# Kernel optimization log

Measured on AMD Instinct MI355X. Metric: run time of the kernel, lower is better.

Reference implementation:

```python
import jax, jax.numpy as jnp
import numpy as np

TEMPERATURE = 8.0  # sqrt(d_k) with d_k = 64
NEG_INF = -1e30    # finite stand-in for -inf; exp() underflows to 0 identically


def _skew(s):
    # Music-Transformer relative-position skew: F.pad(s,(1,0)).view(-1,L+1,L)[:,1:,:]
    B, L, _ = s.shape
    s = jnp.pad(s, ((0, 0), (0, 0), (1, 0)))  # [B, L, L+1]
    return s.reshape(B, L + 1, L)[:, 1:, :]   # [B, L, L]


def setup_inputs() -> dict:
    key = jax.random.key(0)
    kq, kk, kv, ke = jax.random.split(key, 4)
    B, L, D = 16, 2048, 64
    q = jax.random.normal(kq, (B, L, D), dtype=jnp.float32)
    k = jax.random.normal(kk, (B, L, D), dtype=jnp.float32)
    v = jax.random.normal(kv, (B, L, D), dtype=jnp.float32)
    e = jax.random.normal(ke, (B, L, D), dtype=jnp.float32)
    # causal mask (True = masked out), broadcast to batch
    mask = jnp.broadcast_to(jnp.triu(jnp.ones((L, L), dtype=bool), k=1), (B, L, L))
    return {"q": q, "k": k, "v": v, "e": e, "mask": mask}


def reference(q, k, v, e, mask):
    attn = jnp.einsum('bqd,bkd->bqk', q, k)          # q @ k^T
    attn = attn + _skew(jnp.einsum('bqd,bkd->bqk', q, e))
    attn = attn / TEMPERATURE
    attn = jnp.where(mask, NEG_INF, attn)
    attn = jax.nn.softmax(attn, axis=2)
    attn = jnp.where(mask, 0.0, attn)
    # dropout is identity in eval mode
    output = jnp.einsum('bqk,bkd->bqd', attn, v)
    return (output, attn)
```

## Files before the change

### kernel.cpp

```cpp
#include <hip/hip_runtime.h>

typedef unsigned int u32;
typedef __fp16 h2 __attribute__((ext_vector_type(2)));
typedef _Float16 f16x8 __attribute__((ext_vector_type(8)));
typedef float f32x4 __attribute__((ext_vector_type(4)));

#define BB 16
#define LL 2048
#define DD 64
#define RPB 16
#define NTHREADS 512
#define NBLK (LL / RPB)

__device__ __forceinline__ h2 pk(float x, float y) {
#if __has_builtin(__builtin_amdgcn_cvt_pkrtz)
    return __builtin_amdgcn_cvt_pkrtz(x, y);
#else
    h2 r; r.x = (__fp16)x; r.y = (__fp16)y; return r;
#endif
}

union F8U { f16x8 v; h2 p[4]; };
__device__ __forceinline__ f16x8 pack8(float4 a, float4 b) {
    F8U u;
    u.p[0] = pk(a.x, a.y); u.p[1] = pk(a.z, a.w);
    u.p[2] = pk(b.x, b.y); u.p[3] = pk(b.z, b.w);
    return u.v;
}

#define MFMA(A, B, C) __builtin_amdgcn_mfma_f32_16x16x32_f16((A), (B), (C), 0, 0, 0)

__device__ __forceinline__ int swc(int rl, int c) { return c ^ ((rl & 7) << 3); }

__global__ __launch_bounds__(NTHREADS, 4) void attn_fused(
    const float* __restrict__ qg, const float* __restrict__ kg,
    const float* __restrict__ vg, const float* __restrict__ eg,
    float* __restrict__ out_o, float* __restrict__ out_attn)
{
    __shared__ __fp16 S_h[RPB][LL];
    __shared__ float  maxF[RPB][132];
    __shared__ float  linv[RPB];

    const int tid  = threadIdx.x;
    const int wave = tid >> 6;
    const int lane = tid & 63;
    const int o4   = lane >> 4;
    const int lc   = lane & 15;
    const int b    = blockIdx.x / NBLK;
    const int r0   = (blockIdx.x % NBLK) * RPB;
    const int nT   = (r0 >> 6) + 1;

    const float* qb = qg + (size_t)b * LL * DD;
    const float* kb = kg + (size_t)b * LL * DD;
    const float* eb = eg + (size_t)b * LL * DD;
    const float* vb = vg + (size_t)b * LL * DD;

    f16x8 qa0, qa1;
    {
        const float* qr = qb + (size_t)(r0 + lc) * DD + 8 * o4;
        float4 a0 = *(const float4*)(qr);
        float4 a1 = *(const float4*)(qr + 4);
        float4 b0 = *(const float4*)(qr + 32);
        float4 b1 = *(const float4*)(qr + 36);
        qa0 = pack8(a0, a1);
        qa1 = pack8(b0, b1);
    }

    float mx[4] = {-60000.f, -60000.f, -60000.f, -60000.f};

    const int span = r0 + 15 - (wave << 4);
    const int nTw  = (span >= 0) ? ((span >> 7) + 1) : 0;

    for (int t = 0; t < nTw; ++t) {
        const int c0w = (t << 7) + (wave << 4);

        const float* kr = kb + (size_t)(c0w + lc) * DD + 8 * o4;
        float4 k0 = *(const float4*)(kr);
        float4 k1 = *(const float4*)(kr + 4);
        float4 k2 = *(const float4*)(kr + 32);
        float4 k3 = *(const float4*)(kr + 36);

        const int j0w = c0w + 2032 - r0;
        int er0 = j0w + lc;      if (er0 > LL - 1) er0 = LL - 1;
        int er1 = j0w + 16 + lc; if (er1 > LL - 1) er1 = LL - 1;
        const float* e0p = eb + (size_t)er0 * DD + 8 * o4;
        const float* e1p = eb + (size_t)er1 * DD + 8 * o4;
        float4 ea0 = *(const float4*)(e0p);
        float4 ea1 = *(const float4*)(e0p + 4);
        float4 ea2 = *(const float4*)(e0p + 32);
        float4 ea3 = *(const float4*)(e0p + 36);
        float4 eb0 = *(const float4*)(e1p);
        float4 eb1 = *(const float4*)(e1p + 4);
        float4 eb2 = *(const float4*)(e1p + 32);
        float4 eb3 = *(const float4*)(e1p + 36);

        f16x8 kf0 = pack8(k0, k1), kf1 = pack8(k2, k3);
        f16x8 ef00 = pack8(ea0, ea1), ef01 = pack8(ea2, ea3);
        f16x8 ef10 = pack8(eb0, eb1), ef11 = pack8(eb2, eb3);

        const f32x4 z = {0.f, 0.f, 0.f, 0.f};
        f32x4 dk = MFMA(qa0, kf0, z);  dk = MFMA(qa1, kf1, dk);
        f32x4 g0 = MFMA(qa0, ef00, z); g0 = MFMA(qa1, ef01, g0);
        f32x4 g1 = MFMA(qa0, ef10, z); g1 = MFMA(qa1, ef11, g1);

#pragma unroll
        for (int i = 0; i < 4; ++i) {
            const int rl  = 4 * o4 + i;
            const int lj  = lc + 15 - rl;
            const int src = (o4 << 4) | (lj & 15);
            float ga = __shfl(g0[i], src, 64);
            float gb = __shfl(g1[i], src, 64);
            float gv = (lj < 16) ? ga : gb;
            float s = (dk[i] + gv) * 0.125f;
            const int c = c0w + lc;
            if (c > r0 + rl) s = -60000.f;
            mx[i] = fmaxf(mx[i], s);
            S_h[rl][swc(rl, c)] = (__fp16)s;
        }
    }

#pragma unroll
    for (int i = 0; i < 4; ++i)
        maxF[4 * o4 + i][(wave << 4) | lc] = mx[i];
    __syncthreads();

    for (int rr = 0; rr < 2; ++rr) {
        const int rl = (wave << 1) + rr;
        const int r  = r0 + rl;
        float m = fmaxf(maxF[rl][lane], maxF[rl][64 + lane]);
#pragma unroll
        for (int off = 32; off; off >>= 1) m = fmaxf(m, __shfl_xor(m, off, 64));
        float l = 0.f;
        for (int t = 0; t < nT; ++t) {
            const int c  = (t << 6) + lane;
            const int cs = swc(rl, c);
            float p = (c <= r) ? __expf((float)S_h[rl][cs] - m) : 0.f;
            l += p;
            S_h[rl][cs] = (__fp16)p;
        }
#pragma unroll
        for (int off = 32; off; off >>= 1) l += __shfl_xor(l, off, 64);
        const float inv = 1.f / l;
        if (lane == 0) linv[rl] = inv;
        float* arow = out_attn + ((size_t)b * LL + r) * LL;
#pragma unroll 4
        for (int t = 0; t < LL / 64; ++t) {
            const int c = (t << 6) + lane;
            arow[c] = (c <= r) ? (float)S_h[rl][swc(rl, c)] * inv : 0.f;
        }
    }
    __syncthreads();

    const int dw = (wave & 3) << 4;
    const int th = wave >> 2;
    f32x4 acc = {0.f, 0.f, 0.f, 0.f};
    const int koff = o4 << 3;

    for (int t = th; t < nT; t += 2) {
        const int cb = t << 6;
        f16x8 pa0 = *(const f16x8*)&S_h[lc][swc(lc, cb + koff)];
        f16x8 pa1 = *(const f16x8*)&S_h[lc][swc(lc, cb + 32 + koff)];
        const float* vp0 = vb + (size_t)(cb + koff) * DD + dw + lc;
        const float* vp1 = vb + (size_t)(cb + 32 + koff) * DD + dw + lc;
        float a0 = vp0[0],      a1 = vp0[DD],     a2 = vp0[2*DD], a3 = vp0[3*DD];
        float a4 = vp0[4*DD],   a5 = vp0[5*DD],   a6 = vp0[6*DD], a7 = vp0[7*DD];
        float c0 = vp1[0],      c1 = vp1[DD],     c2 = vp1[2*DD], c3 = vp1[3*DD];
        float c4 = vp1[4*DD],   c5 = vp1[5*DD],   c6 = vp1[6*DD], c7 = vp1[7*DD];
        f16x8 vf0 = pack8(make_float4(a0, a1, a2, a3), make_float4(a4, a5, a6, a7));
        f16x8 vf1 = pack8(make_float4(c0, c1, c2, c3), make_float4(c4, c5, c6, c7));
        acc = MFMA(pa0, vf0, acc);
        acc = MFMA(pa1, vf1, acc);
    }

    float* red = &maxF[0][0];
    if (wave >= 4) {
#pragma unroll
        for (int i = 0; i < 4; ++i)
            red[(wave & 3) * 256 + (4 * o4 + i) * 16 + lc] = acc[i];
    }
    __syncthreads();
    if (wave < 4) {
#pragma unroll
        for (int i = 0; i < 4; ++i) {
            const int rl = 4 * o4 + i;
            float oo = acc[i] + red[wave * 256 + rl * 16 + lc];
            out_o[((size_t)b * LL + r0 + rl) * DD + dw + lc] = oo * linv[rl];
        }
    }
}

extern "C" void kernel_launch(void* const* d_in, const int* in_sizes, int n_in,
                              void* d_out, int out_size, void* d_ws, size_t ws_size,
                              hipStream_t stream) {
    const float* q = (const float*)d_in[0];
    const float* k = (const float*)d_in[1];
    const float* v = (const float*)d_in[2];
    const float* e = (const float*)d_in[3];
    float* out_o    = (float*)d_out;
    float* out_attn = out_o + (size_t)BB * LL * DD;

    dim3 grid(BB * NBLK);
    attn_fused<<<grid, NTHREADS, 0, stream>>>(q, k, v, e, out_o, out_attn);
}
```

Before: 651.6 us.

## Replace LDS score row with two-pass online softmax and streamed PV

Drops the full 16x2048 fp16 score buffer in LDS. Pass one computes the scores and keeps a running row max and sum in registers, merging them across waves through small shared arrays. Pass two recomputes the scores, writes the normalized probabilities straight to global memory, and feeds them through a small per-wave LDS tile into PV MFMAs, whose partial outputs are reduced across waves at the end. The masked upper triangle is zeroed with float4 stores, and the block shrinks to 256 threads with higher occupancy. In exchange, the QK and QE MFMAs and the K/E loads run twice, and the V loads are now strided scalar reads per wave.

```diff
diff --git a/kernel.cpp b/kernel.cpp
--- a/kernel.cpp
+++ b/kernel.cpp
@@ -9,7 +9,7 @@
 #define LL 2048
 #define DD 64
 #define RPB 16
-#define NTHREADS 512
+#define NTHREADS 256
 #define NBLK (LL / RPB)
 
 __device__ __forceinline__ h2 pk(float x, float y) {
@@ -27,19 +27,73 @@
     u.p[2] = pk(b.x, b.y); u.p[3] = pk(b.z, b.w);
     return u.v;
 }
+__device__ __forceinline__ f16x8 pack8s(const float* s) {
+    F8U u;
+    u.p[0] = pk(s[0], s[1]); u.p[1] = pk(s[2], s[3]);
+    u.p[2] = pk(s[4], s[5]); u.p[3] = pk(s[6], s[7]);
+    return u.v;
+}
 
 #define MFMA(A, B, C) __builtin_amdgcn_mfma_f32_16x16x32_f16((A), (B), (C), 0, 0, 0)
 
-__device__ __forceinline__ int swc(int rl, int c) { return c ^ ((rl & 7) << 3); }
-
-__global__ __launch_bounds__(NTHREADS, 4) void attn_fused(
+__device__ __forceinline__ void score_quad(
+    int t, int wave, int o4, int lc, int r0,
+    const float* __restrict__ kb, const float* __restrict__ eb,
+    f16x8 qa0, f16x8 qa1, float s[4])
+{
+    const int c0w = (t << 6) + (wave << 4);
+
+    const float* kr = kb + (size_t)(c0w + lc) * DD + 8 * o4;
+    float4 k0 = *(const float4*)(kr);
+    float4 k1 = *(const float4*)(kr + 4);
+    float4 k2 = *(const float4*)(kr + 32);
+    float4 k3 = *(const float4*)(kr + 36);
+
+    const int j0w = c0w + 2032 - r0;
+    int er0 = j0w + lc;      if (er0 > LL - 1) er0 = LL - 1;
+    int er1 = j0w + 16 + lc; if (er1 > LL - 1) er1 = LL - 1;
+    const float* e0p = eb + (size_t)er0 * DD + 8 * o4;
+    const float* e1p = eb + (size_t)er1 * DD + 8 * o4;
+    float4 ea0 = *(const float4*)(e0p);
+    float4 ea1 = *(const float4*)(e0p + 4);
+    float4 ea2 = *(const float4*)(e0p + 32);
+    float4 ea3 = *(const float4*)(e0p + 36);
+    float4 eb0 = *(const float4*)(e1p);
+    float4 eb1 = *(const float4*)(e1p + 4);
+    float4 eb2 = *(const float4*)(e1p + 32);
+    float4 eb3 = *(const float4*)(e1p + 36);
+
+    f16x8 kf0 = pack8(k0, k1), kf1 = pack8(k2, k3);
+    f16x8 ef00 = pack8(ea0, ea1), ef01 = pack8(ea2, ea3);
+    f16x8 ef10 = pack8(eb0, eb1), ef11 = pack8(eb2, eb3);
+
+    const f32x4 z = {0.f, 0.f, 0.f, 0.f};
+    f32x4 dk = MFMA(qa0, kf0, z);  dk = MFMA(qa1, kf1, dk);
+    f32x4 g0 = MFMA(qa0, ef00, z); g0 = MFMA(qa1, ef01, g0);
+    f32x4 g1 = MFMA(qa0, ef10, z); g1 = MFMA(qa1, ef11, g1);
+
+#pragma unroll
+    for (int i = 0; i < 4; ++i) {
+        const int rl  = 4 * o4 + i;
+        const int lj  = lc + 15 - rl;
+        const int src = (o4 << 4) | (lj & 15);
+        float ga = __shfl(g0[i], src, 64);
+        float gb = __shfl(g1[i], src, 64);
+        float gv = (lj < 16) ? ga : gb;
+        float sv = (dk[i] + gv) * 0.125f;
+        if (c0w + lc > r0 + rl) sv = -60000.f;
+        s[i] = sv;
+    }
+}
+
+__global__ __launch_bounds__(NTHREADS, 6) void attn_fused(
     const float* __restrict__ qg, const float* __restrict__ kg,
     const float* __restrict__ vg, const float* __restrict__ eg,
     float* __restrict__ out_o, float* __restrict__ out_attn)
 {
-    __shared__ __fp16 S_h[RPB][LL];
-    __shared__ float  maxF[RPB][132];
-    __shared__ float  linv[RPB];
+    __shared__ __align__(16) __fp16 St[4][2][16][24];
+    __shared__ float Ored[3][16][68];
+    __shared__ float mred[16][4], lred[16][4], mfin[16], linvs[16];
 
     const int tid  = threadIdx.x;
     const int wave = tid >> 6;
@@ -48,12 +102,22 @@
     const int lc   = lane & 15;
     const int b    = blockIdx.x / NBLK;
     const int r0   = (blockIdx.x % NBLK) * RPB;
-    const int nT   = (r0 >> 6) + 1;
-
-    const float* qb = qg + (size_t)b * LL * DD;
-    const float* kb = kg + (size_t)b * LL * DD;
-    const float* eb = eg + (size_t)b * LL * DD;
-    const float* vb = vg + (size_t)b * LL * DD;
+    const size_t bLL = (size_t)b * LL;
+
+    const float* qb = qg + bLL * DD;
+    const float* kb = kg + bLL * DD;
+    const float* eb = eg + bLL * DD;
+    const float* vb = vg + bLL * DD;
+
+    {
+        const int z0 = r0 + RPB;
+        const int nq = (LL - z0) >> 2;
+        const float4 z4 = make_float4(0.f, 0.f, 0.f, 0.f);
+        for (int ri = 0; ri < RPB; ++ri) {
+            float4* zp = (float4*)(out_attn + (bLL + r0 + ri) * LL + z0);
+            for (int i = tid; i < nq; i += NTHREADS) zp[i] = z4;
+        }
+    }
 
     f16x8 qa0, qa1;
     {
@@ -66,126 +130,113 @@
         qa1 = pack8(b0, b1);
     }
 
-    float mx[4] = {-60000.f, -60000.f, -60000.f, -60000.f};
-
     const int span = r0 + 15 - (wave << 4);
-    const int nTw  = (span >= 0) ? ((span >> 7) + 1) : 0;
+    const int nTw  = (span >= 0) ? ((span >> 6) + 1) : 0;
+
+    float mrun[4] = {-60000.f, -60000.f, -60000.f, -60000.f};
+    float lrun[4] = {0.f, 0.f, 0.f, 0.f};
 
     for (int t = 0; t < nTw; ++t) {
-        const int c0w = (t << 7) + (wave << 4);
-
-        const float* kr = kb + (size_t)(c0w + lc) * DD + 8 * o4;
-        float4 k0 = *(const float4*)(kr);
-        float4 k1 = *(const float4*)(kr + 4);
-        float4 k2 = *(const float4*)(kr + 32);
-        float4 k3 = *(const float4*)(kr + 36);
-
-        const int j0w = c0w + 2032 - r0;
-        int er0 = j0w + lc;      if (er0 > LL - 1) er0 = LL - 1;
-        int er1 = j0w + 16 + lc; if (er1 > LL - 1) er1 = LL - 1;
-        const float* e0p = eb + (size_t)er0 * DD + 8 * o4;
-        const float* e1p = eb + (size_t)er1 * DD + 8 * o4;
-        float4 ea0 = *(const float4*)(e0p);
-        float4 ea1 = *(const float4*)(e0p + 4);
-        float4 ea2 = *(const float4*)(e0p + 32);
-        float4 ea3 = *(const float4*)(e0p + 36);
-        float4 eb0 = *(const float4*)(e1p);
-        float4 eb1 = *(const float4*)(e1p + 4);
-        float4 eb2 = *(const float4*)(e1p + 32);
-        float4 eb3 = *(const float4*)(e1p + 36);
-
-        f16x8 kf0 = pack8(k0, k1), kf1 = pack8(k2, k3);
-        f16x8 ef00 = pack8(ea0, ea1), ef01 = pack8(ea2, ea3);
-        f16x8 ef10 = pack8(eb0, eb1), ef11 = pack8(eb2, eb3);
-
-        const f32x4 z = {0.f, 0.f, 0.f, 0.f};
-        f32x4 dk = MFMA(qa0, kf0, z);  dk = MFMA(qa1, kf1, dk);
-        f32x4 g0 = MFMA(qa0, ef00, z); g0 = MFMA(qa1, ef01, g0);
-        f32x4 g1 = MFMA(qa0, ef10, z); g1 = MFMA(qa1, ef11, g1);
-
+        float s[4];
+        score_quad(t, wave, o4, lc, r0, kb, eb, qa0, qa1, s);
 #pragma unroll
         for (int i = 0; i < 4; ++i) {
-            const int rl  = 4 * o4 + i;
-            const int lj  = lc + 15 - rl;
-            const int src = (o4 << 4) | (lj & 15);
-            float ga = __shfl(g0[i], src, 64);
-            float gb = __shfl(g1[i], src, 64);
-            float gv = (lj < 16) ? ga : gb;
-            float s = (dk[i] + gv) * 0.125f;
-            const int c = c0w + lc;
-            if (c > r0 + rl) s = -60000.f;
-            mx[i] = fmaxf(mx[i], s);
-            S_h[rl][swc(rl, c)] = (__fp16)s;
-        }
-    }
-
-#pragma unroll
-    for (int i = 0; i < 4; ++i)
-        maxF[4 * o4 + i][(wave << 4) | lc] = mx[i];
+            float tm = s[i];
+            tm = fmaxf(tm, __shfl_xor(tm, 1, 64));
+            tm = fmaxf(tm, __shfl_xor(tm, 2, 64));
+            tm = fmaxf(tm, __shfl_xor(tm, 4, 64));
+            tm = fmaxf(tm, __shfl_xor(tm, 8, 64));
+            float mn = fmaxf(mrun[i], tm);
+            float sc = __expf(mrun[i] - mn);
+            lrun[i] = lrun[i] * sc + __expf(s[i] - mn);
+            mrun[i] = mn;
+        }
+    }
+#pragma unroll
+    for (int i = 0; i < 4; ++i) {
+        float lt = lrun[i];
+        lt += __shfl_xor(lt, 1, 64);
+        lt += __shfl_xor(lt, 2, 64);
+        lt += __shfl_xor(lt, 4, 64);
+        lt += __shfl_xor(lt, 8, 64);
+        if (lc == 0) { mred[4 * o4 + i][wave] = mrun[i]; lred[4 * o4 + i][wave] = lt; }
+    }
     __syncthreads();
-
-    for (int rr = 0; rr < 2; ++rr) {
-        const int rl = (wave << 1) + rr;
-        const int r  = r0 + rl;
-        float m = fmaxf(maxF[rl][lane], maxF[rl][64 + lane]);
-#pragma unroll
-        for (int off = 32; off; off >>= 1) m = fmaxf(m, __shfl_xor(m, off, 64));
+    if (tid < RPB) {
+        float m = -60000.f;
+#pragma unroll
+        for (int w = 0; w < 4; ++w) m = fmaxf(m, mred[tid][w]);
         float l = 0.f;
-        for (int t = 0; t < nT; ++t) {
-            const int c  = (t << 6) + lane;
-            const int cs = swc(rl, c);
-            float p = (c <= r) ? __expf((float)S_h[rl][cs] - m) : 0.f;
-            l += p;
-            S_h[rl][cs] = (__fp16)p;
-        }
-#pragma unroll
-        for (int off = 32; off; off >>= 1) l += __shfl_xor(l, off, 64);
-        const float inv = 1.f / l;
-        if (lane == 0) linv[rl] = inv;
-        float* arow = out_attn + ((size_t)b * LL + r) * LL;
-#pragma unroll 4
-        for (int t = 0; t < LL / 64; ++t) {
-            const int c = (t << 6) + lane;
-            arow[c] = (c <= r) ? (float)S_h[rl][swc(rl, c)] * inv : 0.f;
-        }
+#pragma unroll
+        for (int w = 0; w < 4; ++w) l += lred[tid][w] * __expf(mred[tid][w] - m);
+        mfin[tid]  = m;
+        linvs[tid] = 1.f / l;
     }
     __syncthreads();
 
-    const int dw = (wave & 3) << 4;
-    const int th = wave >> 2;
-    f32x4 acc = {0.f, 0.f, 0.f, 0.f};
-    const int koff = o4 << 3;
-
-    for (int t = th; t < nT; t += 2) {
-        const int cb = t << 6;
-        f16x8 pa0 = *(const f16x8*)&S_h[lc][swc(lc, cb + koff)];
-        f16x8 pa1 = *(const f16x8*)&S_h[lc][swc(lc, cb + 32 + koff)];
-        const float* vp0 = vb + (size_t)(cb + koff) * DD + dw + lc;
-        const float* vp1 = vb + (size_t)(cb + 32 + koff) * DD + dw + lc;
-        float a0 = vp0[0],      a1 = vp0[DD],     a2 = vp0[2*DD], a3 = vp0[3*DD];
-        float a4 = vp0[4*DD],   a5 = vp0[5*DD],   a6 = vp0[6*DD], a7 = vp0[7*DD];
-        float c0 = vp1[0],      c1 = vp1[DD],     c2 = vp1[2*DD], c3 = vp1[3*DD];
-        float c4 = vp1[4*DD],   c5 = vp1[5*DD],   c6 = vp1[6*DD], c7 = vp1[7*DD];
-        f16x8 vf0 = pack8(make_float4(a0, a1, a2, a3), make_float4(a4, a5, a6, a7));
-        f16x8 vf1 = pack8(make_float4(c0, c1, c2, c3), make_float4(c4, c5, c6, c7));
-        acc = MFMA(pa0, vf0, acc);
-        acc = MFMA(pa1, vf1, acc);
-    }
-
-    float* red = &maxF[0][0];
-    if (wave >= 4) {
-#pragma unroll
-        for (int i = 0; i < 4; ++i)
-            red[(wave & 3) * 256 + (4 * o4 + i) * 16 + lc] = acc[i];
+    float mF[4], iF[4];
+#pragma unroll
+    for (int i = 0; i < 4; ++i) { mF[i] = mfin[4 * o4 + i]; iF[i] = linvs[4 * o4 + i]; }
+
+    f32x4 oacc[4];
+#pragma unroll
+    for (int dc = 0; dc < 4; ++dc) oacc[dc] = (f32x4){0.f, 0.f, 0.f, 0.f};
+
+#define PV_PAIR(CE, CO) do {                                                       \
+        f16x8 pa = *(const f16x8*)&St[wave][o4 >> 1][lc][(o4 & 1) << 3];           \
+        const int vbase = (((o4) < 2) ? (CE) : (CO)) + ((o4 & 1) << 3);            \
+        _Pragma("unroll")                                                          \
+        for (int dc = 0; dc < 4; ++dc) {                                           \
+            const float* vp = vb + (size_t)vbase * DD + dc * 16 + lc;              \
+            float ve[8];                                                           \
+            _Pragma("unroll")                                                      \
+            for (int e = 0; e < 8; ++e) ve[e] = vp[(size_t)e * DD];                \
+            f16x8 vf = pack8s(ve);                                                 \
+            oacc[dc] = MFMA(pa, vf, oacc[dc]);                                     \
+        }                                                                          \
+    } while (0)
+
+    for (int t = 0; t < nTw; ++t) {
+        float s[4];
+        score_quad(t, wave, o4, lc, r0, kb, eb, qa0, qa1, s);
+        const int c = (t << 6) + (wave << 4) + lc;
+        float p[4];
+#pragma unroll
+        for (int i = 0; i < 4; ++i) {
+            p[i] = __expf(s[i] - mF[i]) * iF[i];
+            out_attn[(bLL + r0 + 4 * o4 + i) * LL + c] = p[i];
+            St[wave][t & 1][4 * o4 + i][lc] = (__fp16)p[i];
+        }
+        if (t & 1) {
+            const int ce = ((t - 1) << 6) + (wave << 4);
+            const int co = (t << 6) + (wave << 4);
+            PV_PAIR(ce, co);
+        }
+    }
+    if (nTw & 1) {
+#pragma unroll
+        for (int i = 0; i < 4; ++i) St[wave][1][4 * o4 + i][lc] = (__fp16)0.f;
+        const int ce = ((nTw - 1) << 6) + (wave << 4);
+        PV_PAIR(ce, ce);
+    }
+
+    if (wave > 0) {
+#pragma unroll
+        for (int dc = 0; dc < 4; ++dc)
+#pragma unroll
+            for (int i = 0; i < 4; ++i)
+                Ored[wave - 1][4 * o4 + i][dc * 16 + lc] = oacc[dc][i];
     }
     __syncthreads();
-    if (wave < 4) {
-#pragma unroll
-        for (int i = 0; i < 4; ++i) {
-            const int rl = 4 * o4 + i;
-            float oo = acc[i] + red[wave * 256 + rl * 16 + lc];
-            out_o[((size_t)b * LL + r0 + rl) * DD + dw + lc] = oo * linv[rl];
-        }
+    if (wave == 0) {
+#pragma unroll
+        for (int dc = 0; dc < 4; ++dc)
+#pragma unroll
+            for (int i = 0; i < 4; ++i) {
+                const int rl = 4 * o4 + i, d = dc * 16 + lc;
+                float o = oacc[dc][i] + Ored[0][rl][d] + Ored[1][rl][d] + Ored[2][rl][d];
+                out_o[(bLL + r0 + rl) * DD + d] = o;
+            }
     }
 }
 
```

After: 982.9 us. 1.51x slower.
